# Kernel optimization log

Measured on AMD Instinct MI355X. Metric: run time of the kernel, lower is better.

## Reference

```python
import jax, jax.numpy as jnp
import numpy as np

B, S, D_IN, H, SS, D_OUT = 4, 4096, 2048, 32, 64, 2048


def setup_inputs() -> dict:
    key = jax.random.key(0)
    k1, k2, k3, k4, k5 = jax.random.split(key, 5)
    x = jax.random.normal(k1, (B, S, D_IN), dtype=jnp.float32)
    input_state = jnp.zeros((B, H, SS), dtype=jnp.float32)
    input_weight = jax.random.normal(k2, (H * SS, D_IN), dtype=jnp.float32) * 0.02
    state_weight = jax.random.normal(k3, (H, SS, SS), dtype=jnp.float32) * 0.05
    state_bias = jax.random.normal(k4, (H, SS), dtype=jnp.float32) * 0.02
    output_weight = jax.random.normal(k5, (D_OUT, H * SS), dtype=jnp.float32) * 0.02
    return {
        "x": x,
        "input_state": input_state,
        "input_weight": input_weight,
        "state_weight": state_weight,
        "state_bias": state_bias,
        "output_weight": output_weight,
    }


def reference(x, input_state, input_weight, state_weight, state_bias, output_weight):
    b, s, _ = x.shape
    h, ss, _ = state_weight.shape
    # input projection: [B,S,D_in] -> [B,S,H,Ss], bias folded in once
    hx = jnp.einsum("bsi,oi->bso", x, input_weight).reshape(b, s, h, ss) + state_bias

    def step(y_prev, h_t):
        # y_t = tanh(W_state @ y_{t-1} + x_t)   per head
        y = jnp.tanh(jnp.einsum("hij,bhj->bhi", state_weight, y_prev) + h_t)
        return y, y

    # scan over time axis
    _, ys = jax.lax.scan(step, input_state, jnp.transpose(hx, (1, 0, 2, 3)))
    y = jnp.transpose(ys, (1, 0, 2, 3)).reshape(b, s, h * ss)
    return jnp.einsum("bsk,ok->bso", y, output_weight)
```

## Files before the change

kernel.cpp:

```cpp
#include <hip/hip_runtime.h>
#include <hip/hip_bf16.h>
#include <stdint.h>

#define S_LEN 4096
#define HN    32
#define SSD   64
#define KD    2048
#define MROWS 16384

typedef __attribute__((ext_vector_type(4))) float f32x4;
typedef __attribute__((ext_vector_type(8))) short bf16x8;
typedef __attribute__((ext_vector_type(2))) int i32x2;
typedef __attribute__((ext_vector_type(4))) int i32x4;
typedef __attribute__((ext_vector_type(2))) _Float16 f16x2;
typedef __attribute__((address_space(3))) char as3char;
typedef __attribute__((address_space(1))) char as1char;

__device__ __forceinline__ unsigned short f2bf(float f){
  unsigned int u = __float_as_uint(f);
  u += 0x7FFFu + ((u >> 16) & 1u);
  return (unsigned short)(u >> 16);
}

__device__ __forceinline__ f16x2 bc_h2(int v){
  union { int i; f16x2 h; } u; u.i = v; return u.h;
}

__global__ __launch_bounds__(256) void cvt_bf16_k(const float* __restrict__ src,
                                                  unsigned short* __restrict__ dst){
  int i = (blockIdx.x * 256 + threadIdx.x) * 4;
  float4 v = *(const float4*)(src + i);
  ushort4 r;
  r.x = f2bf(v.x); r.y = f2bf(v.y); r.z = f2bf(v.z); r.w = f2bf(v.w);
  *(ushort4*)(dst + i) = r;
}

__global__ __launch_bounds__(256) void gemm_bf16_k(const unsigned short* __restrict__ A,
                                                   const unsigned short* __restrict__ Bw,
                                                   const float* __restrict__ bias,
                                                   float* __restrict__ C){
  __shared__ short As[2][128*32];
  __shared__ short Bs[2][128*32];
  const int tid  = threadIdx.x;
  const int bn   = blockIdx.x & 15;
  const int bm   = blockIdx.x >> 4;
  const int lane = tid & 63;
  const int wv   = tid >> 6;
  const int wvU  = __builtin_amdgcn_readfirstlane(wv);
  const int wm   = (wv >> 1) * 64;
  const int wn   = (wv & 1) * 64;

  f32x4 acc[4][4];
#pragma unroll
  for (int i=0;i<4;i++)
#pragma unroll
    for (int j=0;j<4;j++)
#pragma unroll
      for (int q=0;q<4;q++) acc[i][j][q] = 0.0f;

  as1char* aG  = (as1char*)A;
  as1char* bG  = (as1char*)Bw;

  const int fr  = lane & 15;
  const int fko = (lane >> 4) * 8;

#define STAGE(bf, kt) { \
    _Pragma("unroll") \
    for (int c=0;c<2;c++){ \
      const int off  = (wvU*2 + c)*1024 + lane*16; \
      const int row  = off >> 6; \
      const int colB = off & 63; \
      __builtin_amdgcn_global_load_lds( \
        (__attribute__((address_space(1))) void*)(aG + (size_t)(bm*128 + row)*4096 + (size_t)(kt)*64 + colB), \
        (__attribute__((address_space(3))) void*)((as3char*)As + (size_t)(bf)*8192 + (wvU*2 + c)*1024), \
        16, 0, 0); \
      __builtin_amdgcn_global_load_lds( \
        (__attribute__((address_space(1))) void*)(bG + (size_t)(bn*128 + row)*4096 + (size_t)(kt)*64 + colB), \
        (__attribute__((address_space(3))) void*)((as3char*)Bs + (size_t)(bf)*8192 + (wvU*2 + c)*1024), \
        16, 0, 0); \
    } }

  STAGE(0, 0)
  __syncthreads();

  int cur = 0;
  for (int kt = 0; kt < KD/32; ++kt){
    if (kt + 1 < KD/32) STAGE(cur^1, kt+1)

    const short* as = &As[cur][0];
    const short* bs = &Bs[cur][0];
    bf16x8 af[4], bq[4];
#pragma unroll
    for (int mt=0; mt<4; mt++) af[mt] = *(const bf16x8*)&as[(wm + mt*16 + fr)*32 + fko];
#pragma unroll
    for (int nt=0; nt<4; nt++) bq[nt] = *(const bf16x8*)&bs[(wn + nt*16 + fr)*32 + fko];
#pragma unroll
    for (int mt=0; mt<4; mt++)
#pragma unroll
      for (int nt=0; nt<4; nt++)
        acc[mt][nt] = __builtin_amdgcn_mfma_f32_16x16x32_bf16(af[mt], bq[nt], acc[mt][nt], 0, 0, 0);

    __syncthreads();
    cur ^= 1;
  }
#undef STAGE

  float bv[4] = {0.f, 0.f, 0.f, 0.f};
  if (bias){
#pragma unroll
    for (int nt=0; nt<4; nt++) bv[nt] = bias[bn*128 + wn + nt*16 + fr];
  }
#pragma unroll
  for (int mt=0; mt<4; mt++)
#pragma unroll
    for (int nt=0; nt<4; nt++){
      const int col = bn*128 + wn + nt*16 + fr;
#pragma unroll
      for (int q=0; q<4; q++){
        const int row = bm*128 + wm + mt*16 + (lane>>4)*4 + q;
        C[(size_t)row*KD + col] = acc[mt][nt][q] + bv[nt];
      }
    }
}

__global__ __attribute__((amdgpu_flat_work_group_size(64, 64)))
__attribute__((amdgpu_waves_per_eu(1, 1)))
void scan_k(const float* __restrict__ hx,
            const float* __restrict__ sw,
            const float* __restrict__ st0,
            unsigned short* __restrict__ ybf){
  const int b = blockIdx.x >> 5, h = blockIdx.x & 31;
  const int lane = threadIdx.x;
  const f32x4* wv = (const f32x4*)(sw + ((size_t)(h*64 + lane))*64);

#define MKP(Q, PA, PB) { f32x4 q_ = wv[Q]; \
    PA = f16x2{(_Float16)q_[0], (_Float16)q_[1]}; \
    PB = f16x2{(_Float16)q_[2], (_Float16)q_[3]}; }
  f16x2 p0,p1,p2,p3,p4,p5,p6,p7,p8,p9,p10,p11,p12,p13,p14,p15,
        p16,p17,p18,p19,p20,p21,p22,p23,p24,p25,p26,p27,p28,p29,p30,p31;
  MKP(0,p0,p1)   MKP(1,p2,p3)   MKP(2,p4,p5)   MKP(3,p6,p7)
  MKP(4,p8,p9)   MKP(5,p10,p11) MKP(6,p12,p13) MKP(7,p14,p15)
  MKP(8,p16,p17) MKP(9,p18,p19) MKP(10,p20,p21)MKP(11,p22,p23)
  MKP(12,p24,p25)MKP(13,p26,p27)MKP(14,p28,p29)MKP(15,p30,p31)
#undef MKP
  asm volatile("" : "+v"(p0),"+v"(p1),"+v"(p2),"+v"(p3),"+v"(p4),"+v"(p5),
                    "+v"(p6),"+v"(p7),"+v"(p8),"+v"(p9),"+v"(p10),"+v"(p11),
                    "+v"(p12),"+v"(p13),"+v"(p14),"+v"(p15));
  asm volatile("" : "+v"(p16),"+v"(p17),"+v"(p18),"+v"(p19),"+v"(p20),"+v"(p21),
                    "+v"(p22),"+v"(p23),"+v"(p24),"+v"(p25),"+v"(p26),"+v"(p27),
                    "+v"(p28),"+v"(p29),"+v"(p30),"+v"(p31));

  __shared__ __align__(16) unsigned short yf16[2][64];
  __shared__ __align__(16) unsigned short ybuf[4][64];

  float y = st0[(b*32 + h)*64 + lane];
  yf16[0][lane] = (unsigned short)__builtin_bit_cast(unsigned short, (_Float16)y);

  const float* hxp = hx + (size_t)b*S_LEN*KD + h*64 + lane;
  unsigned short* const ybase = ybf + (size_t)b*S_LEN*KD + h*64;
  const int srow = lane >> 4;
  const int scol = (lane & 15) << 2;

  float h0 = hxp[0*(size_t)KD], h1 = hxp[1*(size_t)KD],
        h2 = hxp[2*(size_t)KD], h3 = hxp[3*(size_t)KD];

#define DOT4(R, PA,PB,PC,PD) \
    a0 = __builtin_amdgcn_fdot2(PA, bc_h2(R[0]), a0, false); \
    a1 = __builtin_amdgcn_fdot2(PB, bc_h2(R[1]), a1, false); \
    a2 = __builtin_amdgcn_fdot2(PC, bc_h2(R[2]), a2, false); \
    a3 = __builtin_amdgcn_fdot2(PD, bc_h2(R[3]), a3, false);

#define RNN_STEP(H, J, TT, CUR, NXT) { \
    const float hxv = H; \
    { const int tn_ = ((TT) + 4 < S_LEN) ? ((TT) + 4) : (S_LEN - 1); \
      H = hxp[(size_t)tn_ * KD]; } \
    const i32x4* yb4 = (const i32x4*)yf16[CUR];    \
    const i32x4 r0 = yb4[0], r1 = yb4[1], r2 = yb4[2], r3 = yb4[3]; \
    const i32x4 r4 = yb4[4], r5 = yb4[5], r6 = yb4[6], r7 = yb4[7]; \
    float a0=0.f, a1=0.f, a2=0.f, a3=0.f; \
    DOT4(r0, p0,p1,p2,p3)     DOT4(r1, p4,p5,p6,p7) \
    DOT4(r2, p8,p9,p10,p11)   DOT4(r3, p12,p13,p14,p15) \
    DOT4(r4, p16,p17,p18,p19) DOT4(r5, p20,p21,p22,p23) \
    DOT4(r6, p24,p25,p26,p27) DOT4(r7, p28,p29,p30,p31) \
    const float u = (a0 + a1) + (a2 + a3) + hxv; \
    const float e = __expf(2.0f*u); \
    y = 1.0f - 2.0f*__builtin_amdgcn_rcpf(e + 1.0f); \
    yf16[NXT][lane] = (unsigned short)__builtin_bit_cast(unsigned short, (_Float16)y); \
    ybuf[J][lane] = f2bf(y); }

  for (int t = 0; t < S_LEN; t += 4){
    RNN_STEP(h0, 0, t+0, 0, 1)
    RNN_STEP(h1, 1, t+1, 1, 0)
    RNN_STEP(h2, 2, t+2, 0, 1)
    RNN_STEP(h3, 3, t+3, 1, 0)
    const i32x2 v = *(const i32x2*)&ybuf[srow][scol];
    *(i32x2*)(ybase + (size_t)(t + srow)*KD + scol) = v;
  }
#undef RNN_STEP
#undef DOT4
}

extern "C" void kernel_launch(void* const* d_in, const int* in_sizes, int n_in,
                              void* d_out, int out_size, void* d_ws, size_t ws_size,
                              hipStream_t stream) {
  const float* x      = (const float*)d_in[0];
  const float* st0    = (const float*)d_in[1];
  const float* w_in   = (const float*)d_in[2];
  const float* w_st   = (const float*)d_in[3];
  const float* b_st   = (const float*)d_in[4];
  const float* w_out  = (const float*)d_in[5];
  float* out = (float*)d_out;

  const size_t HX_B = (size_t)MROWS * KD * 4;
  const size_t Y_B  = (size_t)MROWS * KD * 2;
  const size_t WO_B = (size_t)KD * KD * 2;
  if (ws_size < HX_B + Y_B + WO_B) return;
  char* ws = (char*)d_ws;
  float*          hx   = (float*)ws;
  unsigned short* ybf  = (unsigned short*)(ws + HX_B);
  unsigned short* wbf  = (unsigned short*)(ws + HX_B + Y_B);

  cvt_bf16_k<<<dim3((MROWS*(size_t)KD)/1024), dim3(256), 0, stream>>>(x, ybf);
  cvt_bf16_k<<<dim3((KD*KD)/1024), dim3(256), 0, stream>>>(w_in, wbf);
  gemm_bf16_k<<<dim3((MROWS/128)*(KD/128)), dim3(256), 0, stream>>>(ybf, wbf, b_st, hx);
  scan_k<<<dim3(128), dim3(64), 0, stream>>>(hx, w_st, st0, ybf);
  cvt_bf16_k<<<dim3((KD*KD)/1024), dim3(256), 0, stream>>>(w_out, wbf);
  gemm_bf16_k<<<dim3((MROWS/128)*(KD/128)), dim3(256), 0, stream>>>(ybf, wbf, nullptr, out);
}
```

Measured before the change: 1.128 ms.

## Store input projection as bf16 and replace GEMM syncthreads with explicit waitcnt barriers

The first GEMM now writes its hx output as bf16 rather than fp32, and the scan kernel reads it as bf16 and widens it to float. This halves the GEMM's write traffic and the scan's per-step global read traffic. The GEMM main loop also swaps __syncthreads for explicit vmcnt/lgkmcnt waits and s_barrier, so the next stage's loads can stay in flight. In exchange, hx carries bf16 precision, and the hand-written waitcnt counts must match the number of outstanding loads.

```diff
diff --git a/kernel.cpp b/kernel.cpp
--- a/kernel.cpp
+++ b/kernel.cpp
@@ -21,7 +21,9 @@
   u += 0x7FFFu + ((u >> 16) & 1u);
   return (unsigned short)(u >> 16);
 }
-
+__device__ __forceinline__ float bf2f_u(unsigned u){
+  return __uint_as_float(u << 16);
+}
 __device__ __forceinline__ f16x2 bc_h2(int v){
   union { int i; f16x2 h; } u; u.i = v; return u.h;
 }
@@ -35,10 +37,11 @@
   *(ushort4*)(dst + i) = r;
 }
 
+template <bool BF16OUT>
 __global__ __launch_bounds__(256) void gemm_bf16_k(const unsigned short* __restrict__ A,
                                                    const unsigned short* __restrict__ Bw,
                                                    const float* __restrict__ bias,
-                                                   float* __restrict__ C){
+                                                   void* __restrict__ Cv){
   __shared__ short As[2][128*32];
   __shared__ short Bs[2][128*32];
   const int tid  = threadIdx.x;
@@ -81,11 +84,17 @@
     } }
 
   STAGE(0, 0)
-  __syncthreads();
 
   int cur = 0;
   for (int kt = 0; kt < KD/32; ++kt){
-    if (kt + 1 < KD/32) STAGE(cur^1, kt+1)
+    if (kt + 1 < KD/32){
+      STAGE(cur^1, kt+1)
+      asm volatile("s_waitcnt vmcnt(4)" ::: "memory");
+    } else {
+      asm volatile("s_waitcnt vmcnt(0)" ::: "memory");
+    }
+    asm volatile("s_barrier" ::: "memory");
+    __builtin_amdgcn_sched_barrier(0);
 
     const short* as = &As[cur][0];
     const short* bs = &Bs[cur][0];
@@ -100,7 +109,7 @@
       for (int nt=0; nt<4; nt++)
         acc[mt][nt] = __builtin_amdgcn_mfma_f32_16x16x32_bf16(af[mt], bq[nt], acc[mt][nt], 0, 0, 0);
 
-    __syncthreads();
+    asm volatile("s_waitcnt lgkmcnt(0)\n\ts_barrier" ::: "memory");
     cur ^= 1;
   }
 #undef STAGE
@@ -118,14 +127,16 @@
 #pragma unroll
       for (int q=0; q<4; q++){
         const int row = bm*128 + wm + mt*16 + (lane>>4)*4 + q;
-        C[(size_t)row*KD + col] = acc[mt][nt][q] + bv[nt];
+        const float v = acc[mt][nt][q] + bv[nt];
+        if constexpr (BF16OUT) ((unsigned short*)Cv)[(size_t)row*KD + col] = f2bf(v);
+        else                   ((float*)Cv)[(size_t)row*KD + col] = v;
       }
     }
 }
 
 __global__ __attribute__((amdgpu_flat_work_group_size(64, 64)))
 __attribute__((amdgpu_waves_per_eu(1, 1)))
-void scan_k(const float* __restrict__ hx,
+void scan_k(const unsigned short* __restrict__ hx,
             const float* __restrict__ sw,
             const float* __restrict__ st0,
             unsigned short* __restrict__ ybf){
@@ -156,13 +167,13 @@
   float y = st0[(b*32 + h)*64 + lane];
   yf16[0][lane] = (unsigned short)__builtin_bit_cast(unsigned short, (_Float16)y);
 
-  const float* hxp = hx + (size_t)b*S_LEN*KD + h*64 + lane;
+  const unsigned short* hxp = hx + (size_t)b*S_LEN*KD + h*64 + lane;
   unsigned short* const ybase = ybf + (size_t)b*S_LEN*KD + h*64;
   const int srow = lane >> 4;
   const int scol = (lane & 15) << 2;
 
-  float h0 = hxp[0*(size_t)KD], h1 = hxp[1*(size_t)KD],
-        h2 = hxp[2*(size_t)KD], h3 = hxp[3*(size_t)KD];
+  unsigned h0 = hxp[0*(size_t)KD], h1 = hxp[1*(size_t)KD],
+           h2 = hxp[2*(size_t)KD], h3 = hxp[3*(size_t)KD];
 
 #define DOT4(R, PA,PB,PC,PD) \
     a0 = __builtin_amdgcn_fdot2(PA, bc_h2(R[0]), a0, false); \
@@ -171,9 +182,9 @@
     a3 = __builtin_amdgcn_fdot2(PD, bc_h2(R[3]), a3, false);
 
 #define RNN_STEP(H, J, TT, CUR, NXT) { \
-    const float hxv = H; \
+    const float hxv = bf2f_u(H);           \
     { const int tn_ = ((TT) + 4 < S_LEN) ? ((TT) + 4) : (S_LEN - 1); \
-      H = hxp[(size_t)tn_ * KD]; } \
+      H = hxp[(size_t)tn_ * KD]; }         \
     const i32x4* yb4 = (const i32x4*)yf16[CUR];    \
     const i32x4 r0 = yb4[0], r1 = yb4[1], r2 = yb4[2], r3 = yb4[3]; \
     const i32x4 r4 = yb4[4], r5 = yb4[5], r6 = yb4[6], r7 = yb4[7]; \
@@ -211,19 +222,19 @@
   const float* w_out  = (const float*)d_in[5];
   float* out = (float*)d_out;
 
-  const size_t HX_B = (size_t)MROWS * KD * 4;
+  const size_t HX_B = (size_t)MROWS * KD * 2;
   const size_t Y_B  = (size_t)MROWS * KD * 2;
   const size_t WO_B = (size_t)KD * KD * 2;
   if (ws_size < HX_B + Y_B + WO_B) return;
   char* ws = (char*)d_ws;
-  float*          hx   = (float*)ws;
+  unsigned short* hxbf = (unsigned short*)ws;
   unsigned short* ybf  = (unsigned short*)(ws + HX_B);
   unsigned short* wbf  = (unsigned short*)(ws + HX_B + Y_B);
 
   cvt_bf16_k<<<dim3((MROWS*(size_t)KD)/1024), dim3(256), 0, stream>>>(x, ybf);
   cvt_bf16_k<<<dim3((KD*KD)/1024), dim3(256), 0, stream>>>(w_in, wbf);
-  gemm_bf16_k<<<dim3((MROWS/128)*(KD/128)), dim3(256), 0, stream>>>(ybf, wbf, b_st, hx);
-  scan_k<<<dim3(128), dim3(64), 0, stream>>>(hx, w_st, st0, ybf);
+  gemm_bf16_k<true><<<dim3((MROWS/128)*(KD/128)), dim3(256), 0, stream>>>(ybf, wbf, b_st, hxbf);
+  scan_k<<<dim3(128), dim3(64), 0, stream>>>(hxbf, w_st, st0, ybf);
   cvt_bf16_k<<<dim3((KD*KD)/1024), dim3(256), 0, stream>>>(w_out, wbf);
-  gemm_bf16_k<<<dim3((MROWS/128)*(KD/128)), dim3(256), 0, stream>>>(ybf, wbf, nullptr, out);
-}
+  gemm_bf16_k<false><<<dim3((MROWS/128)*(KD/128)), dim3(256), 0, stream>>>(ybf, wbf, nullptr, out);
+}
```

After: 1.075 ms. 1.05x faster.
